# Performance work log

Hardware: AMD Instinct MI355X
Metric: run time of the kernel (lower is better)

Reference implementation:

```python
import jax, jax.numpy as jnp
import numpy as np

N_NODES = 100000
N_EDGES = 1600000
MAX_RADIUS = 3.0
NUM_BASIS = 3
SQRT2 = 2.0 ** 0.5
# e3nn soft_one_hot_linspace 'smooth_finite' prefactor
C_SMOOTH = 1.14136 * float(np.exp(2.0))


def _sus(x):
    # smooth unit step: exp(-1/x) for x>0 else 0 (NaN-safe for grad)
    safe = jnp.where(x > 0.0, x, 1.0)
    return jnp.where(x > 0.0, jnp.exp(-1.0 / safe), 0.0)


def radial_embed(d):
    # soft_one_hot_linspace(d, 0, max_radius, 3, basis='smooth_finite', cutoff=True) * sqrt(num_basis)
    values = jnp.linspace(0.0, MAX_RADIUS, NUM_BASIS + 2)[1:-1]  # [3]
    step = MAX_RADIUS / (NUM_BASIS + 1)
    diff = (d[:, None] - values) / step  # [E,3]
    y = C_SMOOTH * _sus(diff + 1.0) * _sus(1.0 - diff)
    return y * (NUM_BASIS ** 0.5)


def fcnet(x, w1, w2):
    # e3nn FullyConnectedNet([3,16,numel], relu): normalized weights, normalize2mom(relu)=sqrt(2)*relu
    h = SQRT2 * jax.nn.relu(x @ (w1 / w1.shape[0] ** 0.5))
    return h @ (w2 / w2.shape[0] ** 0.5)


def reference(pos, feat, edge_src, edge_dst, fc1_w1, fc1_w2, core_w1, core_w2, fc3_w1, fc3_w2, conv_w, conv_b):
    n = pos.shape[0]
    z = edge_src.shape[0] / n  # average num neighbors
    edge_vec = pos[edge_dst] - pos[edge_src]
    d = jnp.sqrt(jnp.sum(edge_vec * edge_vec, axis=1))  # edges are self-loop-free -> d > 0
    emb = radial_embed(d)  # [E,3]

    # NOTE on e3nn math: with input/mid/output parities all even and sh = 0e+1o+2e,
    # the only parity-allowed paths producing nonzero output are the 0e (scalar) paths,
    # which contract against Y_0 = 1 ('component' normalization). The 4x1e block of the
    # mid irreps is identically zero (no parity-allowed path ever populates it), so the
    # math below (scalar block only, with e3nn path weights) is exactly equivalent.
    def conv(x, w1, w2, mul_in, mul_out, path_w):
        # per-edge weights from radial MLP; keep the 0e->0e instruction block
        w = fcnet(emb, w1, w2)[:, : mul_in * mul_out].reshape(-1, mul_in, mul_out)
        msg = path_w * jnp.einsum('euw,eu->ew', w, x[edge_src])
        return jax.ops.segment_sum(msg, edge_dst, num_segments=n) / z ** 0.5

    x = conv(feat, fc1_w1, fc1_w2, 3, 4, (1.0 / 3.0) ** 0.5)  # tp1: fan_in 3*1 -> pw=1/sqrt(3)
    for i in range(3):
        x = conv(x, core_w1[i], core_w2[i], 4, 4, 0.5)  # tp2 0e path: pw=sqrt(1/4)
    x = conv(x, fc3_w1, fc3_w2, 4, 16, 0.5)  # tp3: pw=sqrt(1/4)
    # Conv1d(16, 2, 1) == pointwise linear
    return x @ conv_w.T + conv_b


def setup_inputs():
    key = jax.random.key(0)
    ks = jax.random.split(key, 12)
    pos = jax.random.uniform(ks[0], (N_NODES, 3), dtype=jnp.float32)  # unit box -> all edge lengths < max_radius
    feat = jax.random.normal(ks[1], (N_NODES, 3), dtype=jnp.float32)
    edge_src = jax.random.randint(ks[2], (N_EDGES,), 0, N_NODES, dtype=jnp.int32)
    off = jax.random.randint(ks[3], (N_EDGES,), 1, N_NODES, dtype=jnp.int32)
    edge_dst = ((edge_src + off) % N_NODES).astype(jnp.int32)  # radius_graph has no self-loops
    return {
        'pos': pos,
        'feat': feat,
        'edge_src': edge_src,
        'edge_dst': edge_dst,
        'fc1_w1': jax.random.normal(ks[4], (3, 16), jnp.float32),
        'fc1_w2': jax.random.normal(ks[5], (16, 12), jnp.float32),
        'core_w1': jax.random.normal(ks[6], (3, 3, 16), jnp.float32),
        'core_w2': jax.random.normal(ks[7], (3, 16, 48), jnp.float32),
        'fc3_w1': jax.random.normal(ks[8], (3, 16), jnp.float32),
        'fc3_w2': jax.random.normal(ks[9], (16, 64), jnp.float32),
        'conv_w': jax.random.normal(ks[10], (2, 16), jnp.float32) * 0.25,
        'conv_b': jax.random.normal(ks[11], (2,), jnp.float32) * 0.1,
    }
```

## Files before the change

kernel.cpp:

```cpp
#include <hip/hip_runtime.h>


#define BCAP 4608
#define NBMAX 400

__device__ __forceinline__ float sus_f(float x) {
    return x > 0.0f ? __expf(-1.0f / x) : 0.0f;
}

__device__ __forceinline__ float uload(const float* p) {
    return __uint_as_float(__builtin_amdgcn_readfirstlane(__float_as_uint(*p)));
}

__global__ __launch_bounds__(1024) void k_bin(
    const int* __restrict__ src, const int* __restrict__ dst,
    int* __restrict__ gcur, int* __restrict__ ptmp,
    const float* __restrict__ fc3w2, const float* __restrict__ cw,
    float* __restrict__ gbuf,
    int nedges, int nb)
{
    __shared__ int cnt[NBMAX];
    __shared__ int gb[NBMAX];
    if (threadIdx.x < NBMAX) cnt[threadIdx.x] = 0;
    __syncthreads();

    int base = blockIdx.x * 8192 + threadIdx.x * 8;
    int pk[8]; int bk[8]; short r[8];
    int ss[8], dd[8];
    if (base + 7 < nedges) {
        int4 s0 = *(const int4*)&src[base];
        int4 s1 = *(const int4*)&src[base + 4];
        int4 d0 = *(const int4*)&dst[base];
        int4 d1 = *(const int4*)&dst[base + 4];
        ss[0]=s0.x; ss[1]=s0.y; ss[2]=s0.z; ss[3]=s0.w;
        ss[4]=s1.x; ss[5]=s1.y; ss[6]=s1.z; ss[7]=s1.w;
        dd[0]=d0.x; dd[1]=d0.y; dd[2]=d0.z; dd[3]=d0.w;
        dd[4]=d1.x; dd[5]=d1.y; dd[6]=d1.z; dd[7]=d1.w;
        #pragma unroll
        for (int i = 0; i < 8; ++i) {
            int b = dd[i] >> 8;
            bk[i] = b;
            pk[i] = (ss[i] << 8) | (dd[i] & 255);
            r[i] = (short)atomicAdd(&cnt[b], 1);
        }
    } else {
        #pragma unroll
        for (int i = 0; i < 8; ++i) {
            int e = base + i;
            if (e < nedges) {
                int s = src[e], t = dst[e];
                int b = t >> 8;
                bk[i] = b;
                pk[i] = (s << 8) | (t & 255);
                r[i] = (short)atomicAdd(&cnt[b], 1);
            } else bk[i] = -1;
        }
    }
    __syncthreads();
    if (threadIdx.x < NBMAX && threadIdx.x < nb) {
        int c = cnt[threadIdx.x];
        gb[threadIdx.x] = c > 0 ? atomicAdd(&gcur[threadIdx.x], c) : 0;
    }
    __syncthreads();
    #pragma unroll
    for (int i = 0; i < 8; ++i) {
        if (bk[i] >= 0) {
            int p = gb[bk[i]] + (int)r[i];
            if (p < BCAP)
                ptmp[bk[i] * BCAP + p] = pk[i];
        }
    }

    if (blockIdx.x == 0 && threadIdx.x < 128) {
        int idx = threadIdx.x;
        int k = idx >> 3, u = (idx >> 1) & 3, c = idx & 1;
        float s = 0.0f;
        #pragma unroll
        for (int w = 0; w < 16; ++w)
            s = fmaf(fc3w2[k * 64 + u * 16 + w], cw[c * 16 + w], s);
        gbuf[idx] = s;
    }
}

__global__ __launch_bounds__(1024) void k_build(
    const int* __restrict__ gcur, const int* __restrict__ ptmp,
    const float* __restrict__ pos,
    float4* __restrict__ ebuf, int2* __restrict__ offs2,
    int n, int nb)
{
    int b = blockIdx.x;
    int cnt = gcur[b]; if (cnt > BCAP) cnt = BCAP;
    int t = threadIdx.x;

    __shared__ int stage[BCAP];
    __shared__ int perm[BCAP];
    __shared__ int deg[256];
    __shared__ int loffs[256];
    __shared__ int cur[256];

    const int* tin = ptmp + b * BCAP;
    for (int j = t; j < cnt; j += 1024) stage[j] = tin[j];
    if (t < 256) deg[t] = 0;
    __syncthreads();

    for (int j = t; j < cnt; j += 1024)
        atomicAdd(&deg[stage[j] & 255], 1);
    __syncthreads();

    if (t < 64) {
        int d0 = deg[4 * t + 0], d1 = deg[4 * t + 1];
        int d2 = deg[4 * t + 2], d3 = deg[4 * t + 3];
        int s = d0 + d1 + d2 + d3;
        int x = s;
        #pragma unroll
        for (int off = 1; off < 64; off <<= 1) {
            int y = __shfl_up(x, off);
            if (t >= off) x += y;
        }
        int ex = x - s;
        int e0 = ex, e1 = ex + d0, e2 = e1 + d1, e3 = e2 + d2;
        loffs[4 * t + 0] = e0; cur[4 * t + 0] = e0;
        loffs[4 * t + 1] = e1; cur[4 * t + 1] = e1;
        loffs[4 * t + 2] = e2; cur[4 * t + 2] = e2;
        loffs[4 * t + 3] = e3; cur[4 * t + 3] = e3;
    }
    __syncthreads();

    int nid0 = b << 8;
    {
        int nn = n - nid0; if (nn > 256) nn = 256;
        if (t < nn) {
            int st = b * BCAP + loffs[t];
            offs2[nid0 + t] = make_int2(st, st + deg[t]);
        }
    }

    for (int j = t; j < cnt; j += 1024) {
        int pkd = stage[j];
        perm[atomicAdd(&cur[pkd & 255], 1)] = pkd;
    }
    __syncthreads();

    const float C = 1.14136f * 7.3890560989306495f;
    for (int j = t; j < cnt; j += 1024) {
        int pkd = perm[j];
        int s = pkd >> 8;
        int tt = nid0 | (pkd & 255);
        float dx = pos[3 * tt + 0] - pos[3 * s + 0];
        float dy = pos[3 * tt + 1] - pos[3 * s + 1];
        float dz = pos[3 * tt + 2] - pos[3 * s + 2];
        float d = sqrtf(dx * dx + dy * dy + dz * dz);
        float e0, e1, e2;
        { float f = (d - 0.75f) * (1.0f / 0.75f);
          e0 = C * sus_f(f + 1.0f) * sus_f(1.0f - f); }
        { float f = (d - 1.50f) * (1.0f / 0.75f);
          e1 = C * sus_f(f + 1.0f) * sus_f(1.0f - f); }
        { float f = (d - 2.25f) * (1.0f / 0.75f);
          e2 = C * sus_f(f + 1.0f) * sus_f(1.0f - f); }
        ebuf[(size_t)b * BCAP + j] = make_float4(__int_as_float(s), e0, e1, e2);
    }
}


__global__ __launch_bounds__(256) void k_node_l1(
    const float* __restrict__ feat, const float4* __restrict__ edata,
    const int2* __restrict__ offs2,
    const float* __restrict__ w1, const float* __restrict__ w2,
    float* __restrict__ xout, int n)
{
    __shared__ float lw[16 * 20];
    if (threadIdx.x < 192) {
        int k = threadIdx.x / 12, r = threadIdx.x % 12;
        lw[k * 20 + r] = w2[k * 12 + r];
    }
    __syncthreads();

    int g = blockIdx.x * 256 + threadIdx.x;
    int nd = g >> 2;
    if (nd >= n) return;
    int t = g & 3;

    float w1r[3][16];
    #pragma unroll
    for (int j = 0; j < 3; ++j)
        #pragma unroll
        for (int k = 0; k < 16; ++k) w1r[j][k] = uload(&w1[j * 16 + k]);

    float O[16][3];
    #pragma unroll
    for (int k = 0; k < 16; ++k)
        #pragma unroll
        for (int u = 0; u < 3; ++u) O[k][u] = 0.0f;

    int2 se = offs2[nd];
    int e = se.x + t;
    if (e < se.y) {
        float4 ed = edata[e];
        int e1 = e + 4;
        float4 edn = edata[e1 < se.y ? e1 : e];
        int s = __float_as_int(ed.x);
        float f0 = feat[3 * s + 0], f1 = feat[3 * s + 1], f2 = feat[3 * s + 2];
        while (true) {
            bool more = e1 < se.y;
            int e2 = e1 + 4;
            float4 ed2 = edata[(more && e2 < se.y) ? e2 : e];
            int sn = __float_as_int(edn.x);
            int sp = more ? sn : s;
            float f0n = feat[3 * sp + 0];
            float f1n = feat[3 * sp + 1];
            float f2n = feat[3 * sp + 2];
            #pragma unroll
            for (int k = 0; k < 16; ++k) {
                float a = fmaf(ed.y, w1r[0][k], fmaf(ed.z, w1r[1][k], ed.w * w1r[2][k]));
                float h = a > 0.0f ? a : 0.0f;
                O[k][0] = fmaf(h, f0, O[k][0]);
                O[k][1] = fmaf(h, f1, O[k][1]);
                O[k][2] = fmaf(h, f2, O[k][2]);
            }
            if (!more) break;
            ed = edn; edn = ed2;
            f0 = f0n; f1 = f1n; f2 = f2n;
            e1 = e2;
        }
    }

    float p0 = 0.f, p1 = 0.f, p2 = 0.f, p3 = 0.f;
    #pragma unroll
    for (int k = 0; k < 16; ++k)
        #pragma unroll
        for (int u = 0; u < 3; ++u) {
            const float4 q = *(const float4*)&lw[k * 20 + u * 4];
            float o = O[k][u];
            p0 = fmaf(o, q.x, p0); p1 = fmaf(o, q.y, p1);
            p2 = fmaf(o, q.z, p2); p3 = fmaf(o, q.w, p3);
        }
    p0 += __shfl_xor(p0, 1); p1 += __shfl_xor(p1, 1);
    p2 += __shfl_xor(p2, 1); p3 += __shfl_xor(p3, 1);
    p0 += __shfl_xor(p0, 2); p1 += __shfl_xor(p1, 2);
    p2 += __shfl_xor(p2, 2); p3 += __shfl_xor(p3, 2);
    if (t == 0) {
        const float S = 0.051031036307982884f;
        float4 o; o.x = p0 * S; o.y = p1 * S; o.z = p2 * S; o.w = p3 * S;
        ((float4*)xout)[nd] = o;
    }
}

__global__ __launch_bounds__(256) void k_node_core(
    const float4* __restrict__ xin, const float4* __restrict__ edata,
    const int2* __restrict__ offs2,
    const float* __restrict__ w1, const float* __restrict__ w2,
    float* __restrict__ xout, int n)
{
    __shared__ float lw[16 * 20];
    {
        int idx = threadIdx.x;
        int k = idx >> 4, r = idx & 15;
        lw[k * 20 + r] = w2[k * 48 + r];
    }
    __syncthreads();

    int g = blockIdx.x * 256 + threadIdx.x;
    int nd = g >> 2;
    if (nd >= n) return;
    int t = g & 3;

    float w1r[3][16];
    #pragma unroll
    for (int j = 0; j < 3; ++j)
        #pragma unroll
        for (int k = 0; k < 16; ++k) w1r[j][k] = uload(&w1[j * 16 + k]);

    float O[16][4];
    #pragma unroll
    for (int k = 0; k < 16; ++k)
        #pragma unroll
        for (int u = 0; u < 4; ++u) O[k][u] = 0.0f;

    int2 se = offs2[nd];
    int e = se.x + t;
    if (e < se.y) {
        float4 ed = edata[e];
        int e1 = e + 4;
        float4 edn = edata[e1 < se.y ? e1 : e];
        float4 x = xin[__float_as_int(ed.x)];
        while (true) {
            bool more = e1 < se.y;
            int e2 = e1 + 4;
            float4 ed2 = edata[(more && e2 < se.y) ? e2 : e];
            int sn = __float_as_int(edn.x);
            float4 xn = xin[more ? sn : __float_as_int(ed.x)];
            #pragma unroll
            for (int k = 0; k < 16; ++k) {
                float a = fmaf(ed.y, w1r[0][k], fmaf(ed.z, w1r[1][k], ed.w * w1r[2][k]));
                float h = a > 0.0f ? a : 0.0f;
                O[k][0] = fmaf(h, x.x, O[k][0]);
                O[k][1] = fmaf(h, x.y, O[k][1]);
                O[k][2] = fmaf(h, x.z, O[k][2]);
                O[k][3] = fmaf(h, x.w, O[k][3]);
            }
            if (!more) break;
            ed = edn; edn = ed2; x = xn; e1 = e2;
        }
    }

    float p0 = 0.f, p1 = 0.f, p2 = 0.f, p3 = 0.f;
    #pragma unroll
    for (int k = 0; k < 16; ++k)
        #pragma unroll
        for (int u = 0; u < 4; ++u) {
            const float4 q = *(const float4*)&lw[k * 20 + u * 4];
            float o = O[k][u];
            p0 = fmaf(o, q.x, p0); p1 = fmaf(o, q.y, p1);
            p2 = fmaf(o, q.z, p2); p3 = fmaf(o, q.w, p3);
        }
    p0 += __shfl_xor(p0, 1); p1 += __shfl_xor(p1, 1);
    p2 += __shfl_xor(p2, 1); p3 += __shfl_xor(p3, 1);
    p0 += __shfl_xor(p0, 2); p1 += __shfl_xor(p1, 2);
    p2 += __shfl_xor(p2, 2); p3 += __shfl_xor(p3, 2);
    if (t == 0) {
        const float S = 0.04419417382415922f;
        float4 o; o.x = p0 * S; o.y = p1 * S; o.z = p2 * S; o.w = p3 * S;
        ((float4*)xout)[nd] = o;
    }
}

__global__ __launch_bounds__(256) void k_node_fc3_final(
    const float4* __restrict__ xin, const float4* __restrict__ edata,
    const int2* __restrict__ offs2,
    const float* __restrict__ w1, const float* __restrict__ gbuf,
    const float* __restrict__ cb,
    float* __restrict__ out, int n)
{
    __shared__ float lg[128];
    if (threadIdx.x < 128) lg[threadIdx.x] = gbuf[threadIdx.x];
    __syncthreads();

    int g = blockIdx.x * 256 + threadIdx.x;
    int nd = g >> 2;
    if (nd >= n) return;
    int t = g & 3;

    float w1r[3][16];
    #pragma unroll
    for (int j = 0; j < 3; ++j)
        #pragma unroll
        for (int k = 0; k < 16; ++k) w1r[j][k] = uload(&w1[j * 16 + k]);

    float O[16][4];
    #pragma unroll
    for (int k = 0; k < 16; ++k)
        #pragma unroll
        for (int u = 0; u < 4; ++u) O[k][u] = 0.0f;

    int2 se = offs2[nd];
    int e = se.x + t;
    if (e < se.y) {
        float4 ed = edata[e];
        int e1 = e + 4;
        float4 edn = edata[e1 < se.y ? e1 : e];
        float4 x = xin[__float_as_int(ed.x)];
        while (true) {
            bool more = e1 < se.y;
            int e2 = e1 + 4;
            float4 ed2 = edata[(more && e2 < se.y) ? e2 : e];
            int sn = __float_as_int(edn.x);
            float4 xn = xin[more ? sn : __float_as_int(ed.x)];
            #pragma unroll
            for (int k = 0; k < 16; ++k) {
                float a = fmaf(ed.y, w1r[0][k], fmaf(ed.z, w1r[1][k], ed.w * w1r[2][k]));
                float h = a > 0.0f ? a : 0.0f;
                O[k][0] = fmaf(h, x.x, O[k][0]);
                O[k][1] = fmaf(h, x.y, O[k][1]);
                O[k][2] = fmaf(h, x.z, O[k][2]);
                O[k][3] = fmaf(h, x.w, O[k][3]);
            }
            if (!more) break;
            ed = edn; edn = ed2; x = xn; e1 = e2;
        }
    }

    float a0 = 0.f, a1 = 0.f;
    #pragma unroll
    for (int k = 0; k < 16; ++k)
        #pragma unroll
        for (int u = 0; u < 4; ++u) {
            float o = O[k][u];
            const float2 q = *(const float2*)&lg[(k * 4 + u) * 2];
            a0 = fmaf(o, q.x, a0);
            a1 = fmaf(o, q.y, a1);
        }
    a0 += __shfl_xor(a0, 1); a1 += __shfl_xor(a1, 1);
    a0 += __shfl_xor(a0, 2); a1 += __shfl_xor(a1, 2);
    if (t == 0) {
        const float S = 0.04419417382415922f;
        float2 o; o.x = fmaf(a0, S, cb[0]); o.y = fmaf(a1, S, cb[1]);
        ((float2*)out)[nd] = o;
    }
}


extern "C" void kernel_launch(void* const* d_in, const int* in_sizes, int n_in,
                              void* d_out, int out_size, void* d_ws, size_t ws_size,
                              hipStream_t stream) {
    const float* pos     = (const float*)d_in[0];
    const float* feat    = (const float*)d_in[1];
    const int*   esrc    = (const int*)d_in[2];
    const int*   edst    = (const int*)d_in[3];
    const float* fc1_w1  = (const float*)d_in[4];
    const float* fc1_w2  = (const float*)d_in[5];
    const float* core_w1 = (const float*)d_in[6];
    const float* core_w2 = (const float*)d_in[7];
    const float* fc3_w1  = (const float*)d_in[8];
    const float* fc3_w2  = (const float*)d_in[9];
    const float* conv_w  = (const float*)d_in[10];
    const float* conv_b  = (const float*)d_in[11];
    float* out = (float*)d_out;

    const int E = in_sizes[2];
    const int N = in_sizes[0] / 3;
    const int nb = (N + 255) >> 8;

    float4* ebuf = (float4*)d_ws;
    int* ptmp  = (int*)(ebuf + (size_t)nb * BCAP);
    float* xa  = (float*)(ptmp + (size_t)nb * BCAP);
    float* xb  = xa + (size_t)4 * N;
    int2* offs2 = (int2*)(xb + (size_t)4 * N);
    int* gcur  = (int*)(offs2 + N);
    float* gbuf = (float*)(gcur + ((nb + 3) & ~3));

    int g4 = (4 * N + 255) / 256;

    hipMemsetAsync(gcur, 0, (size_t)nb * sizeof(int), stream);
    k_bin<<<(E + 8191) / 8192, 1024, 0, stream>>>(esrc, edst, gcur, ptmp,
                                                  fc3_w2, conv_w, gbuf, E, nb);
    k_build<<<nb, 1024, 0, stream>>>(gcur, ptmp, pos, ebuf, offs2, N, nb);

    k_node_l1<<<g4, 256, 0, stream>>>(feat, ebuf, offs2, fc1_w1, fc1_w2, xa, N);
    k_node_core<<<g4, 256, 0, stream>>>((const float4*)xa, ebuf, offs2,
                                        core_w1 + 0, core_w2 + 0, xb, N);
    k_node_core<<<g4, 256, 0, stream>>>((const float4*)xb, ebuf, offs2,
                                        core_w1 + 48, core_w2 + 768, xa, N);
    k_node_core<<<g4, 256, 0, stream>>>((const float4*)xa, ebuf, offs2,
                                        core_w1 + 96, core_w2 + 1536, xb, N);
    k_node_fc3_final<<<g4, 256, 0, stream>>>((const float4*)xb, ebuf, offs2,
                                             fc3_w1, gbuf, conv_b, out, N);
}
```

Baseline: 209.8 us.

## Stage binned edges in shared memory for coalesced global scatter

The binning kernel now takes an exclusive prefix scan of the per-bin counts, writes each packed edge into a bin-sorted local array in LDS, and builds a slot-to-bin map. Threads then write the sorted entries to the global bins contiguously, replacing random per-edge scattered stores with runs of consecutive addresses. The cost is about 48KB of extra LDS per block (which can limit occupancy), an extra barrier, and a serial loop that fills the map for each bin.

```diff
diff --git a/kernel.cpp b/kernel.cpp
--- a/kernel.cpp
+++ b/kernel.cpp
@@ -21,10 +21,16 @@
 {
     __shared__ int cnt[NBMAX];
     __shared__ int gb[NBMAX];
-    if (threadIdx.x < NBMAX) cnt[threadIdx.x] = 0;
-    __syncthreads();
-
-    int base = blockIdx.x * 8192 + threadIdx.x * 8;
+    __shared__ int lscan[NBMAX];
+    __shared__ int tot;
+    __shared__ unsigned short map[8192];
+    __shared__ int lpk[8192];
+
+    int t = threadIdx.x;
+    if (t < NBMAX) cnt[t] = 0;
+    __syncthreads();
+
+    int base = blockIdx.x * 8192 + t * 8;
     int pk[8]; int bk[8]; short r[8];
     int ss[8], dd[8];
     if (base + 7 < nedges) {
@@ -48,31 +54,65 @@
         for (int i = 0; i < 8; ++i) {
             int e = base + i;
             if (e < nedges) {
-                int s = src[e], t = dst[e];
-                int b = t >> 8;
+                int s = src[e], tt = dst[e];
+                int b = tt >> 8;
                 bk[i] = b;
-                pk[i] = (s << 8) | (t & 255);
+                pk[i] = (s << 8) | (tt & 255);
                 r[i] = (short)atomicAdd(&cnt[b], 1);
             } else bk[i] = -1;
         }
     }
     __syncthreads();
-    if (threadIdx.x < NBMAX && threadIdx.x < nb) {
-        int c = cnt[threadIdx.x];
-        gb[threadIdx.x] = c > 0 ? atomicAdd(&gcur[threadIdx.x], c) : 0;
-    }
-    __syncthreads();
+
+    if (t < 64) {
+        int bs = t * 7;
+        int c[7]; int s = 0;
+        #pragma unroll
+        for (int i = 0; i < 7; ++i) {
+            int idx = bs + i;
+            c[i] = (idx < NBMAX) ? cnt[idx] : 0;
+            s += c[i];
+        }
+        int x = s;
+        #pragma unroll
+        for (int off = 1; off < 64; off <<= 1) {
+            int y = __shfl_up(x, off);
+            if (t >= off) x += y;
+        }
+        int run = x - s;
+        #pragma unroll
+        for (int i = 0; i < 7; ++i) {
+            int idx = bs + i;
+            if (idx < NBMAX) lscan[idx] = run;
+            run += c[i];
+        }
+        if (t == 63) tot = run;
+    }
+    if (t < NBMAX && t < nb) {
+        int c = cnt[t];
+        gb[t] = c > 0 ? atomicAdd(&gcur[t], c) : 0;
+    }
+    __syncthreads();
+
     #pragma unroll
     for (int i = 0; i < 8; ++i) {
-        if (bk[i] >= 0) {
-            int p = gb[bk[i]] + (int)r[i];
-            if (p < BCAP)
-                ptmp[bk[i] * BCAP + p] = pk[i];
-        }
-    }
-
-    if (blockIdx.x == 0 && threadIdx.x < 128) {
-        int idx = threadIdx.x;
+        if (bk[i] >= 0) lpk[lscan[bk[i]] + (int)r[i]] = pk[i];
+    }
+    if (t < NBMAX && t < nb) {
+        int beg = lscan[t], end = beg + cnt[t];
+        for (int j = beg; j < end; ++j) map[j] = (unsigned short)t;
+    }
+    __syncthreads();
+
+    for (int j = t; j < tot; j += 1024) {
+        int b = map[j];
+        int p = gb[b] + (j - lscan[b]);
+        if (p < BCAP)
+            ptmp[b * BCAP + p] = lpk[j];
+    }
+
+    if (blockIdx.x == 0 && t < 128) {
+        int idx = t;
         int k = idx >> 3, u = (idx >> 1) & 3, c = idx & 1;
         float s = 0.0f;
         #pragma unroll
```

New measurement: 207.3 us. No clear change (-1.2%).
